# Optimization experiments

Measured on AMD Instinct MI355X. Metric: run time of the kernel, lower is better.

## Reference

```python
import jax, jax.numpy as jnp
import numpy as np

CHANNELS = 256
TEMPERATURE = 0.1
VAR_LAMBDA = 0.001
N = 4096


def _pairwise_sq_dist(x, y):
    xx = jnp.sum(x * x, axis=-1)[:, None]
    yy = jnp.sum(y * y, axis=-1)[None, :]
    xy = jnp.einsum('ic,jc->ij', x, y)
    return xx + yy - 2.0 * xy


def _tcc_loss(emb_a, emb_b, idxes):
    scale = 1.0 / (CHANNELS * TEMPERATURE)
    sim_ab = -_pairwise_sq_dist(emb_a, emb_b) * scale            # [Na, Nb]
    softmaxed_sim_ab = jax.nn.softmax(sim_ab, axis=-1)
    soft_nn = softmaxed_sim_ab @ emb_b                            # [Na, C]
    sim_ba = -_pairwise_sq_dist(soft_nn, emb_a) * scale           # [Na, Na]
    beta = jax.nn.softmax(sim_ba, axis=-1)
    preds = jnp.sum(beta * idxes, axis=-1, keepdims=True)         # [Na, 1]
    pred_var = jnp.sum((idxes - preds) ** 2 * beta, axis=1)       # [Na]
    pred_var_log = jnp.log(pred_var)
    squared_error = (idxes - jnp.squeeze(preds, -1)) ** 2
    return jnp.sum(jnp.exp(-pred_var_log) * squared_error + VAR_LAMBDA * pred_var_log)


def setup_inputs() -> dict:
    key = jax.random.key(0)
    k1, k2 = jax.random.split(key)
    emb_a = jax.random.normal(k1, (1, N, CHANNELS), dtype=jnp.float32)
    emb_b = jax.random.normal(k2, (1, N, CHANNELS), dtype=jnp.float32)
    idx_a = jnp.arange(N, dtype=jnp.float32)
    idx_b = jnp.arange(N, dtype=jnp.float32)
    return {"emb_a": emb_a, "emb_b": emb_b, "idx_a": idx_a, "idx_b": idx_b}


def reference(emb_a, emb_b, idx_a, idx_b):
    a = jnp.squeeze(emb_a, 0)
    b = jnp.squeeze(emb_b, 0)
    loss_ab = _tcc_loss(a, b, idx_a)
    loss_ba = _tcc_loss(b, a, idx_b)
    return (loss_ab + loss_ba) / (a.shape[0] + b.shape[0])
```

## Files before the change

### kernel.cpp

```cpp
#include <hip/hip_runtime.h>

#define NTOT 4096
#define CH 256
#define SCALE 0.0390625f
#define LAM 0.001f

typedef unsigned short u16;
typedef __attribute__((ext_vector_type(8))) short short8;
typedef __attribute__((ext_vector_type(4))) float floatx4;

__device__ __forceinline__ float wave_sum64(float v) {
  #pragma unroll
  for (int o = 32; o; o >>= 1) v += __shfl_down(v, o, 64);
  return v;
}
__device__ __forceinline__ u16 f2bf(float f) {
  unsigned u = __float_as_uint(f);
  u += 0x7fffu + ((u >> 16) & 1u);
  return (u16)(u >> 16);
}
__device__ __forceinline__ float bf2f(u16 h) {
  return __uint_as_float(((unsigned)h) << 16);
}
__device__ __forceinline__ void gload_lds(const u16* g, void* l) {
  __builtin_amdgcn_global_load_lds((const __attribute__((address_space(1))) void*)g,
                                   (__attribute__((address_space(3))) void*)l, 16, 0, 0);
}
__device__ __forceinline__ void mm4x4(const short8 (&av)[4], const short8 (&bv)[4],
                                      floatx4 (&acc)[4][4]) {
  #pragma unroll
  for (int m = 0; m < 4; ++m)
    #pragma unroll
    for (int n = 0; n < 4; ++n)
      acc[m][n] = __builtin_amdgcn_mfma_f32_16x16x32_bf16(av[m], bv[n], acc[m][n], 0, 0, 0);
}

__global__ __launch_bounds__(64) void cvt_norm_k(const float* __restrict__ a,
                                                 const float* __restrict__ b,
                                                 u16* __restrict__ ab, u16* __restrict__ bb,
                                                 float* __restrict__ na, float* __restrict__ nb) {
  int row = blockIdx.x;
  const float* src; u16* dst; float* nd;
  if (row < NTOT) { src = a; dst = ab; nd = na; }
  else { row -= NTOT; src = b; dst = bb; nd = nb; }
  const float4 v = *reinterpret_cast<const float4*>(src + (size_t)row * CH + threadIdx.x * 4);
  const u16 h0 = f2bf(v.x), h1 = f2bf(v.y), h2 = f2bf(v.z), h3 = f2bf(v.w);
  uint2 st;
  st.x = (unsigned)h0 | ((unsigned)h1 << 16);
  st.y = (unsigned)h2 | ((unsigned)h3 << 16);
  *reinterpret_cast<uint2*>(dst + (size_t)row * CH + threadIdx.x * 4) = st;
  const float f0 = bf2f(h0), f1 = bf2f(h1), f2 = bf2f(h2), f3 = bf2f(h3);
  float s = f0 * f0 + f1 * f1 + f2 * f2 + f3 * f3;
  s = wave_sum64(s);
  if (threadIdx.x == 0) nd[row] = s;
}

__global__ __launch_bounds__(256) void transpose2_k(const u16* __restrict__ ab,
                                                    const u16* __restrict__ bb,
                                                    u16* __restrict__ at, u16* __restrict__ bt) {
  const u16* __restrict__ src = blockIdx.z ? bb : ab;
  u16* __restrict__ dst = blockIdx.z ? bt : at;
  __shared__ u16 t[32][33];
  const int bx = blockIdx.x * 32, by = blockIdx.y * 32;
  const int lx = threadIdx.x & 31, ly = threadIdx.x >> 5;
  #pragma unroll
  for (int i = 0; i < 32; i += 8)
    t[ly + i][lx] = src[(size_t)(by + ly + i) * CH + bx + lx];
  __syncthreads();
  #pragma unroll
  for (int i = 0; i < 32; i += 8)
    dst[(size_t)(bx + ly + i) * NTOT + by + lx] = t[lx][ly + i];
}

__global__ __launch_bounds__(256, 2) void gemm_exp_k(const u16* __restrict__ abf,
                                                     const u16* __restrict__ bbf,
                                                     const float* __restrict__ na,
                                                     const float* __restrict__ nb,
                                                     u16* __restrict__ E,
                                                     float* __restrict__ dnp) {
  const int dir = blockIdx.z;
  const u16* __restrict__ A = dir ? bbf : abf;
  const u16* __restrict__ B = dir ? abf : bbf;
  const float* __restrict__ ny = dir ? na : nb;
  E += (size_t)dir * NTOT * NTOT;
  dnp += (size_t)dir * NTOT * 64;

  __shared__ u16 As[2][128][64];
  __shared__ u16 Bs[2][128][64];
  const int tid = threadIdx.x, wid = tid >> 6, lane = tid & 63;
  const int bn = blockIdx.x * 128, bm = blockIdx.y * 128;
  const int wr = (wid >> 1) * 64, wc = (wid & 1) * 64;
  const int lr = lane & 15;

  auto stage = [&](int t, int bi) {
    const int k0 = t * 64;
    #pragma unroll
    for (int i = 0; i < 4; ++i) {
      const int lb = (wid + 4 * i) * 1024;
      const int db = lb + lane * 16;
      const int r = db >> 7;
      const int cb = (db & 127) ^ ((r & 7) << 4);
      gload_lds(A + (size_t)(bm + r) * CH + k0 + (cb >> 1), (char*)&As[bi][0][0] + lb);
      gload_lds(B + (size_t)(bn + r) * CH + k0 + (cb >> 1), (char*)&Bs[bi][0][0] + lb);
    }
  };

  floatx4 acc[4][4] = {};
  stage(0, 0);
  asm volatile("s_waitcnt vmcnt(0)" ::: "memory");
  __builtin_amdgcn_s_barrier();
  #pragma unroll
  for (int t = 0; t < 4; ++t) {
    if (t < 3) stage(t + 1, (t + 1) & 1);
    const int bi = t & 1;
    const char* Ab = (const char*)&As[bi][0][0];
    const char* Bb = (const char*)&Bs[bi][0][0];
    #pragma unroll
    for (int ks = 0; ks < 2; ++ks) {
      const int ob = ks * 64 + (lane >> 4) * 16;
      short8 af[4], bfr[4];
      #pragma unroll
      for (int m = 0; m < 4; ++m) {
        const int row = wr + m * 16 + lr;
        af[m] = *reinterpret_cast<const short8*>(Ab + row * 128 + (ob ^ ((row & 7) << 4)));
      }
      #pragma unroll
      for (int n = 0; n < 4; ++n) {
        const int row = wc + n * 16 + lr;
        bfr[n] = *reinterpret_cast<const short8*>(Bb + row * 128 + (ob ^ ((row & 7) << 4)));
      }
      mm4x4(af, bfr, acc);
    }
    if (t < 3) {
      asm volatile("s_waitcnt vmcnt(0)" ::: "memory");
      __builtin_amdgcn_s_barrier();
    }
  }
  float nyv[4];
  #pragma unroll
  for (int n = 0; n < 4; ++n) nyv[n] = ny[bn + wc + n * 16 + lr];
  float rowsum[4][4] = {};
  #pragma unroll
  for (int m = 0; m < 4; ++m) {
    const int rowb = bm + wr + m * 16 + (lane >> 4) * 4;
    #pragma unroll
    for (int n = 0; n < 4; ++n) {
      const int col = bn + wc + n * 16 + lr;
      #pragma unroll
      for (int r = 0; r < 4; ++r) {
        const float w = __expf((2.f * acc[m][n][r] - nyv[n]) * SCALE);
        E[(size_t)(rowb + r) * NTOT + col] = f2bf(w);
        rowsum[m][r] += w;
      }
    }
  }
  #pragma unroll
  for (int m = 0; m < 4; ++m) {
    const int rowb = bm + wr + m * 16 + (lane >> 4) * 4;
    #pragma unroll
    for (int r = 0; r < 4; ++r) {
      float s = rowsum[m][r];
      #pragma unroll
      for (int o = 1; o < 16; o <<= 1) s += __shfl_xor(s, o, 64);
      if (lr == 0) dnp[(size_t)(rowb + r) * 64 + blockIdx.x * 2 + (wid & 1)] = s;
    }
  }
}

__global__ __launch_bounds__(256, 2) void gemm_qp_k(const u16* __restrict__ E,
                                                    const u16* __restrict__ att,
                                                    const u16* __restrict__ btt,
                                                    float* __restrict__ Qp) {
  const int dir = blockIdx.z >> 2, kz = blockIdx.z & 3;
  const u16* __restrict__ A = E + (size_t)dir * NTOT * NTOT;
  const u16* __restrict__ B = dir ? att : btt;
  float* __restrict__ C = Qp + (size_t)dir * 4 * NTOT * CH + (size_t)kz * NTOT * CH;
  const int k0base = kz * (NTOT / 4);

  __shared__ u16 As[2][128][64];
  __shared__ u16 Bs[2][128][64];
  const int tid = threadIdx.x, wid = tid >> 6, lane = tid & 63;
  const int bn = blockIdx.x * 128, bm = blockIdx.y * 128;
  const int wr = (wid >> 1) * 64, wc = (wid & 1) * 64;
  const int lr = lane & 15;

  auto stage = [&](int t, int bi) {
    const int k0 = k0base + t * 64;
    #pragma unroll
    for (int i = 0; i < 4; ++i) {
      const int lb = (wid + 4 * i) * 1024;
      const int db = lb + lane * 16;
      const int r = db >> 7;
      const int cb = (db & 127) ^ ((r & 7) << 4);
      gload_lds(A + (size_t)(bm + r) * NTOT + k0 + (cb >> 1), (char*)&As[bi][0][0] + lb);
      gload_lds(B + (size_t)(bn + r) * NTOT + k0 + (cb >> 1), (char*)&Bs[bi][0][0] + lb);
    }
  };

  floatx4 acc[4][4] = {};
  stage(0, 0);
  asm volatile("s_waitcnt vmcnt(0)" ::: "memory");
  __builtin_amdgcn_s_barrier();
  for (int t = 0; t < 16; ++t) {
    if (t < 15) stage(t + 1, (t + 1) & 1);
    const int bi = t & 1;
    const char* Ab = (const char*)&As[bi][0][0];
    const char* Bb = (const char*)&Bs[bi][0][0];
    #pragma unroll
    for (int ks = 0; ks < 2; ++ks) {
      const int ob = ks * 64 + (lane >> 4) * 16;
      short8 af[4], bfr[4];
      #pragma unroll
      for (int m = 0; m < 4; ++m) {
        const int row = wr + m * 16 + lr;
        af[m] = *reinterpret_cast<const short8*>(Ab + row * 128 + (ob ^ ((row & 7) << 4)));
      }
      #pragma unroll
      for (int n = 0; n < 4; ++n) {
        const int row = wc + n * 16 + lr;
        bfr[n] = *reinterpret_cast<const short8*>(Bb + row * 128 + (ob ^ ((row & 7) << 4)));
      }
      mm4x4(af, bfr, acc);
    }
    asm volatile("s_waitcnt vmcnt(0)" ::: "memory");
    __builtin_amdgcn_s_barrier();
  }
  #pragma unroll
  for (int m = 0; m < 4; ++m) {
    const int row = bm + wr + m * 16 + (lane >> 4) * 4;
    #pragma unroll
    for (int n = 0; n < 4; ++n) {
      const int col = bn + wc + n * 16 + lr;
      #pragma unroll
      for (int r = 0; r < 4; ++r)
        C[(size_t)(row + r) * CH + col] = acc[m][n][r];
    }
  }
}

__global__ __launch_bounds__(256) void reduce_q_k(const float* __restrict__ Qp,
                                                  const float* __restrict__ dnp,
                                                  u16* __restrict__ Qb) {
  const int dir = blockIdx.z;
  Qp += (size_t)dir * 4 * NTOT * CH;
  dnp += (size_t)dir * NTOT * 64;
  Qb += (size_t)dir * NTOT * CH;
  const int row = blockIdx.x, tid = threadIdx.x;
  __shared__ float sdn;
  if (tid < 64) {
    float s = dnp[(size_t)row * 64 + tid];
    s = wave_sum64(s);
    if (tid == 0) sdn = 1.0f / s;
  }
  __syncthreads();
  const float rdn = sdn;
  const size_t o = (size_t)row * CH + tid;
  const size_t st = (size_t)NTOT * CH;
  const float q = (Qp[o] + Qp[o + st] + Qp[o + 2 * st] + Qp[o + 3 * st]) * rdn;
  Qb[o] = f2bf(q);
}

__global__ __launch_bounds__(256, 2) void flash_stats_k(const u16* __restrict__ Qball,
                                                        const u16* __restrict__ abf,
                                                        const u16* __restrict__ bbf,
                                                        const float* __restrict__ na,
                                                        const float* __restrict__ nb,
                                                        const float* __restrict__ idxa,
                                                        const float* __restrict__ idxb,
                                                        float4* __restrict__ statsp) {
  const int dir = blockIdx.z;
  const u16* __restrict__ Qb = Qball + (size_t)dir * NTOT * CH;
  const u16* __restrict__ X = dir ? bbf : abf;
  const float* __restrict__ nx = dir ? nb : na;
  const float* __restrict__ idx = dir ? idxb : idxa;
  statsp += (size_t)dir * NTOT * 32;

  __shared__ u16 As[2][128][64];
  __shared__ u16 Bs[2][128][64];
  const int tid = threadIdx.x, wid = tid >> 6, lane = tid & 63;
  const int bm = blockIdx.y * 128;
  const int jbase = blockIdx.x * 256;
  const int wr = (wid >> 1) * 64, wc = (wid & 1) * 64;
  const int lr = lane & 15;

  auto stage = [&](int t, int bi) {
    const int k0 = (t & 3) * 64;
    const int bn = jbase + (t >> 2) * 128;
    #pragma unroll
    for (int i = 0; i < 4; ++i) {
      const int lb = (wid + 4 * i) * 1024;
      const int db = lb + lane * 16;
      const int r = db >> 7;
      const int cb = (db & 127) ^ ((r & 7) << 4);
      gload_lds(Qb + (size_t)(bm + r) * CH + k0 + (cb >> 1), (char*)&As[bi][0][0] + lb);
      gload_lds(X + (size_t)(bn + r) * CH + k0 + (cb >> 1), (char*)&Bs[bi][0][0] + lb);
    }
  };

  float cen[4][4];
  #pragma unroll
  for (int m = 0; m < 4; ++m) {
    const int rowb = bm + wr + m * 16 + (lane >> 4) * 4;
    #pragma unroll
    for (int r = 0; r < 4; ++r) cen[m][r] = idx[rowb + r];
  }
  float s0[4][4] = {}, s1[4][4] = {}, s2[4][4] = {};
  floatx4 acc[4][4] = {};

  stage(0, 0);
  asm volatile("s_waitcnt vmcnt(0)" ::: "memory");
  __builtin_amdgcn_s_barrier();
  #pragma unroll
  for (int t = 0; t < 8; ++t) {
    if (t < 7) stage(t + 1, (t + 1) & 1);
    const int bi = t & 1;
    const char* Ab = (const char*)&As[bi][0][0];
    const char* Bb = (const char*)&Bs[bi][0][0];
    #pragma unroll
    for (int ks = 0; ks < 2; ++ks) {
      const int ob = ks * 64 + (lane >> 4) * 16;
      short8 af[4], bfr[4];
      #pragma unroll
      for (int m = 0; m < 4; ++m) {
        const int row = wr + m * 16 + lr;
        af[m] = *reinterpret_cast<const short8*>(Ab + row * 128 + (ob ^ ((row & 7) << 4)));
      }
      #pragma unroll
      for (int n = 0; n < 4; ++n) {
        const int row = wc + n * 16 + lr;
        bfr[n] = *reinterpret_cast<const short8*>(Bb + row * 128 + (ob ^ ((row & 7) << 4)));
      }
      mm4x4(af, bfr, acc);
    }
    if ((t & 3) == 3) {
      const int bn = jbase + (t >> 2) * 128;
      #pragma unroll
      for (int n = 0; n < 4; ++n) {
        const int col = bn + wc + n * 16 + lr;
        const float nxv = nx[col];
        const float iv = idx[col];
        #pragma unroll
        for (int m = 0; m < 4; ++m) {
          #pragma unroll
          for (int r = 0; r < 4; ++r) {
            const float w = __expf((2.f * acc[m][n][r] - nxv) * SCALE);
            const float d = iv - cen[m][r];
            s0[m][r] += w;
            s1[m][r] += w * d;
            s2[m][r] += w * d * d;
            acc[m][n][r] = 0.f;
          }
        }
      }
    }
    if (t < 7) {
      asm volatile("s_waitcnt vmcnt(0)" ::: "memory");
      __builtin_amdgcn_s_barrier();
    }
  }
  #pragma unroll
  for (int m = 0; m < 4; ++m) {
    const int rowb = bm + wr + m * 16 + (lane >> 4) * 4;
    #pragma unroll
    for (int r = 0; r < 4; ++r) {
      float a = s0[m][r], b = s1[m][r], c = s2[m][r];
      #pragma unroll
      for (int o = 1; o < 16; o <<= 1) {
        a += __shfl_xor(a, o, 64);
        b += __shfl_xor(b, o, 64);
        c += __shfl_xor(c, o, 64);
      }
      if (lr == 0)
        statsp[(size_t)(rowb + r) * 32 + blockIdx.x * 2 + (wid & 1)] = make_float4(a, b, c, 0.f);
    }
  }
}

__global__ __launch_bounds__(256) void stats_combine_k(const float4* __restrict__ statsp,
                                                       float* __restrict__ terms) {
  const int row = blockIdx.x * 256 + threadIdx.x;
  float S0 = 0.f, S1 = 0.f, S2 = 0.f;
  #pragma unroll
  for (int p = 0; p < 32; ++p) {
    const float4 v = statsp[(size_t)row * 32 + p];
    S0 += v.x; S1 += v.y; S2 += v.z;
  }
  const float mu = S1 / S0;
  const float var = S2 / S0 - mu * mu;
  terms[row] = mu * mu / var + LAM * logf(var);
}

__global__ __launch_bounds__(256) void final_reduce_k(const float* __restrict__ terms,
                                                      float* __restrict__ out) {
  float s = 0.f;
  for (int i = threadIdx.x; i < 2 * NTOT; i += 256) s += terms[i];
  __shared__ float red[4];
  s = wave_sum64(s);
  if ((threadIdx.x & 63) == 0) red[threadIdx.x >> 6] = s;
  __syncthreads();
  if (threadIdx.x == 0) out[0] = (red[0] + red[1] + red[2] + red[3]) * (1.0f / (2.0f * NTOT));
}

extern "C" void kernel_launch(void* const* d_in, const int* in_sizes, int n_in,
                              void* d_out, int out_size, void* d_ws, size_t ws_size,
                              hipStream_t stream) {
  const float* a    = (const float*)d_in[0];
  const float* b    = (const float*)d_in[1];
  const float* idxa = (const float*)d_in[2];
  const float* idxb = (const float*)d_in[3];
  float* out = (float*)d_out;
  char* ws = (char*)d_ws;

  size_t off = 0;
  u16*    E    = (u16*)(ws + off);    off += 2 * (size_t)NTOT * NTOT * 2;
  float*  Qp   = (float*)(ws + off);  off += 2 * 4 * (size_t)NTOT * CH * 4;
  u16*    Qb   = (u16*)(ws + off);    off += 2 * (size_t)NTOT * CH * 2;
  u16*    abf  = (u16*)(ws + off);    off += (size_t)NTOT * CH * 2;
  u16*    bbf  = (u16*)(ws + off);    off += (size_t)NTOT * CH * 2;
  u16*    att  = (u16*)(ws + off);    off += (size_t)NTOT * CH * 2;
  u16*    btt  = (u16*)(ws + off);    off += (size_t)NTOT * CH * 2;
  float*  na   = (float*)(ws + off);  off += (size_t)NTOT * 4;
  float*  nb   = (float*)(ws + off);  off += (size_t)NTOT * 4;
  float*  dnp  = (float*)(ws + off);  off += 2 * (size_t)NTOT * 64 * 4;
  float4* stp  = (float4*)(ws + off); off += 2 * (size_t)NTOT * 32 * 16;
  float*  terms = (float*)(ws + off);

  cvt_norm_k<<<2 * NTOT, 64, 0, stream>>>(a, b, abf, bbf, na, nb);
  transpose2_k<<<dim3(CH / 32, NTOT / 32, 2), 256, 0, stream>>>(abf, bbf, att, btt);
  gemm_exp_k<<<dim3(NTOT / 128, NTOT / 128, 2), 256, 0, stream>>>(abf, bbf, na, nb, E, dnp);
  gemm_qp_k<<<dim3(CH / 128, NTOT / 128, 8), 256, 0, stream>>>(E, att, btt, Qp);
  reduce_q_k<<<dim3(NTOT, 1, 2), 256, 0, stream>>>(Qp, dnp, Qb);
  flash_stats_k<<<dim3(16, NTOT / 128, 2), 256, 0, stream>>>(Qb, abf, bbf, na, nb,
                                                             idxa, idxb, stp);
  stats_combine_k<<<2 * NTOT / 256, 256, 0, stream>>>(stp, terms);
  final_reduce_k<<<1, 256, 0, stream>>>(terms, out);
}
```

Baseline: 137.1 us.

## Enlarge GEMM tiles to 256x256 with 8 waves and remap qp grid

gemm_exp_k and flash_stats_k now use 512-thread blocks on 256x256 output tiles, with each wave holding 128x64 of the output (8x4 MFMA accumulators). This cuts redundant global/LDS loads per FLOP. flash_stats now computes a single 256-column tile per block instead of two sequential 128-column tiles, which doubles its stats partials to 64 per row. gemm_qp_k uses a flattened 1D grid with the dir/kz index in the low bits so consecutive blocks spread across splits. The trade-off is higher register pressure (128 accumulator floats), 64KB of LDS per block, and fewer blocks per wave of launches.

```diff
diff --git a/kernel.cpp b/kernel.cpp
--- a/kernel.cpp
+++ b/kernel.cpp
@@ -26,14 +26,7 @@
   __builtin_amdgcn_global_load_lds((const __attribute__((address_space(1))) void*)g,
                                    (__attribute__((address_space(3))) void*)l, 16, 0, 0);
 }
-__device__ __forceinline__ void mm4x4(const short8 (&av)[4], const short8 (&bv)[4],
-                                      floatx4 (&acc)[4][4]) {
-  #pragma unroll
-  for (int m = 0; m < 4; ++m)
-    #pragma unroll
-    for (int n = 0; n < 4; ++n)
-      acc[m][n] = __builtin_amdgcn_mfma_f32_16x16x32_bf16(av[m], bv[n], acc[m][n], 0, 0, 0);
-}
+__device__ __forceinline__ int swz128(int row) { return (row & 7) << 4; }
 
 __global__ __launch_bounds__(64) void cvt_norm_k(const float* __restrict__ a,
                                                  const float* __restrict__ b,
@@ -72,40 +65,41 @@
     dst[(size_t)(bx + ly + i) * NTOT + by + lx] = t[lx][ly + i];
 }
 
-__global__ __launch_bounds__(256, 2) void gemm_exp_k(const u16* __restrict__ abf,
+__global__ __launch_bounds__(512, 2) void gemm_exp_k(const u16* __restrict__ abf,
                                                      const u16* __restrict__ bbf,
                                                      const float* __restrict__ na,
                                                      const float* __restrict__ nb,
                                                      u16* __restrict__ E,
                                                      float* __restrict__ dnp) {
-  const int dir = blockIdx.z;
+  const int bx = blockIdx.x, by = blockIdx.y, dir = blockIdx.z;
   const u16* __restrict__ A = dir ? bbf : abf;
   const u16* __restrict__ B = dir ? abf : bbf;
   const float* __restrict__ ny = dir ? na : nb;
   E += (size_t)dir * NTOT * NTOT;
   dnp += (size_t)dir * NTOT * 64;
 
-  __shared__ u16 As[2][128][64];
-  __shared__ u16 Bs[2][128][64];
+  __shared__ u16 As[2][256][64];
+  __shared__ u16 Bs[2][256][64];
   const int tid = threadIdx.x, wid = tid >> 6, lane = tid & 63;
-  const int bn = blockIdx.x * 128, bm = blockIdx.y * 128;
-  const int wr = (wid >> 1) * 64, wc = (wid & 1) * 64;
-  const int lr = lane & 15;
+  const int bm = by * 256, bn = bx * 256;
+  const int wr = (wid >> 2) * 128;
+  const int wc = (wid & 3) * 64;
+  const int lr = lane & 15, g = lane >> 4;
 
   auto stage = [&](int t, int bi) {
     const int k0 = t * 64;
     #pragma unroll
     for (int i = 0; i < 4; ++i) {
-      const int lb = (wid + 4 * i) * 1024;
+      const int lb = (wid + 8 * i) * 1024;
       const int db = lb + lane * 16;
       const int r = db >> 7;
-      const int cb = (db & 127) ^ ((r & 7) << 4);
+      const int cb = (db & 127) ^ swz128(r);
       gload_lds(A + (size_t)(bm + r) * CH + k0 + (cb >> 1), (char*)&As[bi][0][0] + lb);
       gload_lds(B + (size_t)(bn + r) * CH + k0 + (cb >> 1), (char*)&Bs[bi][0][0] + lb);
     }
   };
 
-  floatx4 acc[4][4] = {};
+  floatx4 acc[8][4] = {};
   stage(0, 0);
   asm volatile("s_waitcnt vmcnt(0)" ::: "memory");
   __builtin_amdgcn_s_barrier();
@@ -117,19 +111,23 @@
     const char* Bb = (const char*)&Bs[bi][0][0];
     #pragma unroll
     for (int ks = 0; ks < 2; ++ks) {
-      const int ob = ks * 64 + (lane >> 4) * 16;
-      short8 af[4], bfr[4];
-      #pragma unroll
-      for (int m = 0; m < 4; ++m) {
+      const int ob = ks * 64 + g * 16;
+      short8 af[8], bfr[4];
+      #pragma unroll
+      for (int m = 0; m < 8; ++m) {
         const int row = wr + m * 16 + lr;
-        af[m] = *reinterpret_cast<const short8*>(Ab + row * 128 + (ob ^ ((row & 7) << 4)));
+        af[m] = *reinterpret_cast<const short8*>(Ab + row * 128 + (ob ^ swz128(row)));
       }
       #pragma unroll
       for (int n = 0; n < 4; ++n) {
         const int row = wc + n * 16 + lr;
-        bfr[n] = *reinterpret_cast<const short8*>(Bb + row * 128 + (ob ^ ((row & 7) << 4)));
-      }
-      mm4x4(af, bfr, acc);
+        bfr[n] = *reinterpret_cast<const short8*>(Bb + row * 128 + (ob ^ swz128(row)));
+      }
+      #pragma unroll
+      for (int m = 0; m < 8; ++m)
+        #pragma unroll
+        for (int n = 0; n < 4; ++n)
+          acc[m][n] = __builtin_amdgcn_mfma_f32_16x16x32_bf16(af[m], bfr[n], acc[m][n], 0, 0, 0);
     }
     if (t < 3) {
       asm volatile("s_waitcnt vmcnt(0)" ::: "memory");
@@ -139,10 +137,10 @@
   float nyv[4];
   #pragma unroll
   for (int n = 0; n < 4; ++n) nyv[n] = ny[bn + wc + n * 16 + lr];
-  float rowsum[4][4] = {};
-  #pragma unroll
-  for (int m = 0; m < 4; ++m) {
-    const int rowb = bm + wr + m * 16 + (lane >> 4) * 4;
+  #pragma unroll
+  for (int m = 0; m < 8; ++m) {
+    const int rowb = bm + wr + m * 16 + g * 4;
+    float rowsum[4] = {};
     #pragma unroll
     for (int n = 0; n < 4; ++n) {
       const int col = bn + wc + n * 16 + lr;
@@ -150,19 +148,15 @@
       for (int r = 0; r < 4; ++r) {
         const float w = __expf((2.f * acc[m][n][r] - nyv[n]) * SCALE);
         E[(size_t)(rowb + r) * NTOT + col] = f2bf(w);
-        rowsum[m][r] += w;
-      }
-    }
-  }
-  #pragma unroll
-  for (int m = 0; m < 4; ++m) {
-    const int rowb = bm + wr + m * 16 + (lane >> 4) * 4;
+        rowsum[r] += w;
+      }
+    }
     #pragma unroll
     for (int r = 0; r < 4; ++r) {
-      float s = rowsum[m][r];
+      float s = rowsum[r];
       #pragma unroll
       for (int o = 1; o < 16; o <<= 1) s += __shfl_xor(s, o, 64);
-      if (lr == 0) dnp[(size_t)(rowb + r) * 64 + blockIdx.x * 2 + (wid & 1)] = s;
+      if (lr == 0) dnp[(size_t)(rowb + r) * 64 + bx * 4 + (wid & 3)] = s;
     }
   }
 }
@@ -171,7 +165,12 @@
                                                     const u16* __restrict__ att,
                                                     const u16* __restrict__ btt,
                                                     float* __restrict__ Qp) {
-  const int dir = blockIdx.z >> 2, kz = blockIdx.z & 3;
+  const int wg = blockIdx.x;
+  const int dk = wg & 7;
+  const int j = wg >> 3;
+  const int dir = dk >> 2, kz = dk & 3;
+  const int bxi = j & 1, byi = j >> 1;
+
   const u16* __restrict__ A = E + (size_t)dir * NTOT * NTOT;
   const u16* __restrict__ B = dir ? att : btt;
   float* __restrict__ C = Qp + (size_t)dir * 4 * NTOT * CH + (size_t)kz * NTOT * CH;
@@ -180,7 +179,7 @@
   __shared__ u16 As[2][128][64];
   __shared__ u16 Bs[2][128][64];
   const int tid = threadIdx.x, wid = tid >> 6, lane = tid & 63;
-  const int bn = blockIdx.x * 128, bm = blockIdx.y * 128;
+  const int bn = bxi * 128, bm = byi * 128;
   const int wr = (wid >> 1) * 64, wc = (wid & 1) * 64;
   const int lr = lane & 15;
 
@@ -191,7 +190,7 @@
       const int lb = (wid + 4 * i) * 1024;
       const int db = lb + lane * 16;
       const int r = db >> 7;
-      const int cb = (db & 127) ^ ((r & 7) << 4);
+      const int cb = (db & 127) ^ swz128(r);
       gload_lds(A + (size_t)(bm + r) * NTOT + k0 + (cb >> 1), (char*)&As[bi][0][0] + lb);
       gload_lds(B + (size_t)(bn + r) * NTOT + k0 + (cb >> 1), (char*)&Bs[bi][0][0] + lb);
     }
@@ -213,14 +212,18 @@
       #pragma unroll
       for (int m = 0; m < 4; ++m) {
         const int row = wr + m * 16 + lr;
-        af[m] = *reinterpret_cast<const short8*>(Ab + row * 128 + (ob ^ ((row & 7) << 4)));
+        af[m] = *reinterpret_cast<const short8*>(Ab + row * 128 + (ob ^ swz128(row)));
       }
       #pragma unroll
       for (int n = 0; n < 4; ++n) {
         const int row = wc + n * 16 + lr;
-        bfr[n] = *reinterpret_cast<const short8*>(Bb + row * 128 + (ob ^ ((row & 7) << 4)));
-      }
-      mm4x4(af, bfr, acc);
+        bfr[n] = *reinterpret_cast<const short8*>(Bb + row * 128 + (ob ^ swz128(row)));
+      }
+      #pragma unroll
+      for (int m = 0; m < 4; ++m)
+        #pragma unroll
+        for (int n = 0; n < 4; ++n)
+          acc[m][n] = __builtin_amdgcn_mfma_f32_16x16x32_bf16(af[m], bfr[n], acc[m][n], 0, 0, 0);
     }
     asm volatile("s_waitcnt vmcnt(0)" ::: "memory");
     __builtin_amdgcn_s_barrier();
@@ -260,7 +263,7 @@
   Qb[o] = f2bf(q);
 }
 
-__global__ __launch_bounds__(256, 2) void flash_stats_k(const u16* __restrict__ Qball,
+__global__ __launch_bounds__(512, 2) void flash_stats_k(const u16* __restrict__ Qball,
                                                         const u16* __restrict__ abf,
                                                         const u16* __restrict__ bbf,
                                                         const float* __restrict__ na,
@@ -268,110 +271,103 @@
                                                         const float* __restrict__ idxa,
                                                         const float* __restrict__ idxb,
                                                         float4* __restrict__ statsp) {
-  const int dir = blockIdx.z;
+  const int bx = blockIdx.x, by = blockIdx.y, dir = blockIdx.z;
   const u16* __restrict__ Qb = Qball + (size_t)dir * NTOT * CH;
   const u16* __restrict__ X = dir ? bbf : abf;
   const float* __restrict__ nx = dir ? nb : na;
   const float* __restrict__ idx = dir ? idxb : idxa;
-  statsp += (size_t)dir * NTOT * 32;
-
-  __shared__ u16 As[2][128][64];
-  __shared__ u16 Bs[2][128][64];
+  statsp += (size_t)dir * NTOT * 64;
+
+  __shared__ u16 As[2][256][64];
+  __shared__ u16 Bs[2][256][64];
   const int tid = threadIdx.x, wid = tid >> 6, lane = tid & 63;
-  const int bm = blockIdx.y * 128;
-  const int jbase = blockIdx.x * 256;
-  const int wr = (wid >> 1) * 64, wc = (wid & 1) * 64;
-  const int lr = lane & 15;
+  const int bm = by * 256, bn = bx * 256;
+  const int wr = (wid >> 2) * 128;
+  const int wc = (wid & 3) * 64;
+  const int lr = lane & 15, g = lane >> 4;
 
   auto stage = [&](int t, int bi) {
-    const int k0 = (t & 3) * 64;
-    const int bn = jbase + (t >> 2) * 128;
+    const int k0 = t * 64;
     #pragma unroll
     for (int i = 0; i < 4; ++i) {
-      const int lb = (wid + 4 * i) * 1024;
+      const int lb = (wid + 8 * i) * 1024;
       const int db = lb + lane * 16;
       const int r = db >> 7;
-      const int cb = (db & 127) ^ ((r & 7) << 4);
+      const int cb = (db & 127) ^ swz128(r);
       gload_lds(Qb + (size_t)(bm + r) * CH + k0 + (cb >> 1), (char*)&As[bi][0][0] + lb);
       gload_lds(X + (size_t)(bn + r) * CH + k0 + (cb >> 1), (char*)&Bs[bi][0][0] + lb);
     }
   };
 
-  float cen[4][4];
-  #pragma unroll
-  for (int m = 0; m < 4; ++m) {
-    const int rowb = bm + wr + m * 16 + (lane >> 4) * 4;
-    #pragma unroll
-    for (int r = 0; r < 4; ++r) cen[m][r] = idx[rowb + r];
-  }
-  float s0[4][4] = {}, s1[4][4] = {}, s2[4][4] = {};
-  floatx4 acc[4][4] = {};
-
+  floatx4 acc[8][4] = {};
   stage(0, 0);
   asm volatile("s_waitcnt vmcnt(0)" ::: "memory");
   __builtin_amdgcn_s_barrier();
   #pragma unroll
-  for (int t = 0; t < 8; ++t) {
-    if (t < 7) stage(t + 1, (t + 1) & 1);
+  for (int t = 0; t < 4; ++t) {
+    if (t < 3) stage(t + 1, (t + 1) & 1);
     const int bi = t & 1;
     const char* Ab = (const char*)&As[bi][0][0];
     const char* Bb = (const char*)&Bs[bi][0][0];
     #pragma unroll
     for (int ks = 0; ks < 2; ++ks) {
-      const int ob = ks * 64 + (lane >> 4) * 16;
-      short8 af[4], bfr[4];
-      #pragma unroll
-      for (int m = 0; m < 4; ++m) {
+      const int ob = ks * 64 + g * 16;
+      short8 af[8], bfr[4];
+      #pragma unroll
+      for (int m = 0; m < 8; ++m) {
         const int row = wr + m * 16 + lr;
-        af[m] = *reinterpret_cast<const short8*>(Ab + row * 128 + (ob ^ ((row & 7) << 4)));
+        af[m] = *reinterpret_cast<const short8*>(Ab + row * 128 + (ob ^ swz128(row)));
       }
       #pragma unroll
       for (int n = 0; n < 4; ++n) {
         const int row = wc + n * 16 + lr;
-        bfr[n] = *reinterpret_cast<const short8*>(Bb + row * 128 + (ob ^ ((row & 7) << 4)));
-      }
-      mm4x4(af, bfr, acc);
-    }
-    if ((t & 3) == 3) {
-      const int bn = jbase + (t >> 2) * 128;
-      #pragma unroll
-      for (int n = 0; n < 4; ++n) {
-        const int col = bn + wc + n * 16 + lr;
-        const float nxv = nx[col];
-        const float iv = idx[col];
+        bfr[n] = *reinterpret_cast<const short8*>(Bb + row * 128 + (ob ^ swz128(row)));
+      }
+      #pragma unroll
+      for (int m = 0; m < 8; ++m)
         #pragma unroll
-        for (int m = 0; m < 4; ++m) {
-          #pragma unroll
-          for (int r = 0; r < 4; ++r) {
-            const float w = __expf((2.f * acc[m][n][r] - nxv) * SCALE);
-            const float d = iv - cen[m][r];
-            s0[m][r] += w;
-            s1[m][r] += w * d;
-            s2[m][r] += w * d * d;
-            acc[m][n][r] = 0.f;
-          }
-        }
-      }
-    }
-    if (t < 7) {
+        for (int n = 0; n < 4; ++n)
+          acc[m][n] = __builtin_amdgcn_mfma_f32_16x16x32_bf16(af[m], bfr[n], acc[m][n], 0, 0, 0);
+    }
+    if (t < 3) {
       asm volatile("s_waitcnt vmcnt(0)" ::: "memory");
       __builtin_amdgcn_s_barrier();
     }
   }
-  #pragma unroll
-  for (int m = 0; m < 4; ++m) {
-    const int rowb = bm + wr + m * 16 + (lane >> 4) * 4;
+  float nxv[4], iv[4];
+  #pragma unroll
+  for (int n = 0; n < 4; ++n) {
+    const int col = bn + wc + n * 16 + lr;
+    nxv[n] = nx[col];
+    iv[n] = idx[col];
+  }
+  #pragma unroll
+  for (int m = 0; m < 8; ++m) {
+    const int rowb = bm + wr + m * 16 + g * 4;
+    float s0[4] = {}, s1[4] = {}, s2[4] = {};
     #pragma unroll
     for (int r = 0; r < 4; ++r) {
-      float a = s0[m][r], b = s1[m][r], c = s2[m][r];
+      const float cen = idx[rowb + r];
+      #pragma unroll
+      for (int n = 0; n < 4; ++n) {
+        const float w = __expf((2.f * acc[m][n][r] - nxv[n]) * SCALE);
+        const float d = iv[n] - cen;
+        s0[r] += w;
+        s1[r] += w * d;
+        s2[r] += w * d * d;
+      }
+    }
+    #pragma unroll
+    for (int r = 0; r < 4; ++r) {
+      float av = s0[r], bv = s1[r], cv = s2[r];
       #pragma unroll
       for (int o = 1; o < 16; o <<= 1) {
-        a += __shfl_xor(a, o, 64);
-        b += __shfl_xor(b, o, 64);
-        c += __shfl_xor(c, o, 64);
+        av += __shfl_xor(av, o, 64);
+        bv += __shfl_xor(bv, o, 64);
+        cv += __shfl_xor(cv, o, 64);
       }
       if (lr == 0)
-        statsp[(size_t)(rowb + r) * 32 + blockIdx.x * 2 + (wid & 1)] = make_float4(a, b, c, 0.f);
+        statsp[(size_t)(rowb + r) * 64 + bx * 4 + (wid & 3)] = make_float4(av, bv, cv, 0.f);
     }
   }
 }
@@ -381,8 +377,8 @@
   const int row = blockIdx.x * 256 + threadIdx.x;
   float S0 = 0.f, S1 = 0.f, S2 = 0.f;
   #pragma unroll
-  for (int p = 0; p < 32; ++p) {
-    const float4 v = statsp[(size_t)row * 32 + p];
+  for (int p = 0; p < 64; ++p) {
+    const float4 v = statsp[(size_t)row * 64 + p];
     S0 += v.x; S1 += v.y; S2 += v.z;
   }
   const float mu = S1 / S0;
@@ -422,16 +418,15 @@
   float*  na   = (float*)(ws + off);  off += (size_t)NTOT * 4;
   float*  nb   = (float*)(ws + off);  off += (size_t)NTOT * 4;
   float*  dnp  = (float*)(ws + off);  off += 2 * (size_t)NTOT * 64 * 4;
-  float4* stp  = (float4*)(ws + off); off += 2 * (size_t)NTOT * 32 * 16;
+  float4* stp  = (float4*)(ws + off); off += 2 * (size_t)NTOT * 64 * 16;
   float*  terms = (float*)(ws + off);
 
   cvt_norm_k<<<2 * NTOT, 64, 0, stream>>>(a, b, abf, bbf, na, nb);
   transpose2_k<<<dim3(CH / 32, NTOT / 32, 2), 256, 0, stream>>>(abf, bbf, att, btt);
-  gemm_exp_k<<<dim3(NTOT / 128, NTOT / 128, 2), 256, 0, stream>>>(abf, bbf, na, nb, E, dnp);
-  gemm_qp_k<<<dim3(CH / 128, NTOT / 128, 8), 256, 0, stream>>>(E, att, btt, Qp);
+  gemm_exp_k<<<dim3(16, 16, 2), 512, 0, stream>>>(abf, bbf, na, nb, E, dnp);
+  gemm_qp_k<<<512, 256, 0, stream>>>(E, att, btt, Qp);
   reduce_q_k<<<dim3(NTOT, 1, 2), 256, 0, stream>>>(Qp, dnp, Qb);
-  flash_stats_k<<<dim3(16, NTOT / 128, 2), 256, 0, stream>>>(Qb, abf, bbf, na, nb,
-                                                             idxa, idxb, stp);
+  flash_stats_k<<<dim3(16, 16, 2), 512, 0, stream>>>(Qb, abf, bbf, na, nb, idxa, idxb, stp);
   stats_combine_k<<<2 * NTOT / 256, 256, 0, stream>>>(stp, terms);
   final_reduce_k<<<1, 256, 0, stream>>>(terms, out);
 }
```

Measured after the change: 140.6 us. 1.03x slower.
